# Kernel tuning notes

Measured on AMD Instinct MI355X. Metric: run time of the kernel, lower is better.

## Reference

```python
import jax, jax.numpy as jnp
import numpy as np

B, L, D, H, R = 2, 2048, 1024, 16, 32
DH = D // H
LORA_SCALE = 64.0 / 32.0  # alpha / rank


def _ln(x, w, b):
    mu = jnp.mean(x, axis=-1, keepdims=True)
    xc = x - mu
    var = jnp.mean(xc * xc, axis=-1, keepdims=True)
    y = xc * jax.lax.rsqrt(var + 1e-5) * w
    return y + b if b is not None else y


def _rotate_half(x):
    x1, x2 = jnp.split(x, 2, axis=-1)
    return jnp.concatenate([-x2, x1], axis=-1)


def _apply_rotary(q, k):
    # q, k: [B, L, H, DH]
    seqlen = q.shape[1]
    inv_freq = 1.0 / (10000.0 ** (jnp.arange(0, DH, 2, dtype=jnp.float32) / DH))
    t = jnp.arange(seqlen, dtype=jnp.float32)
    freqs = t[:, None] * inv_freq[None, :]           # [L, DH/2]
    emb = jnp.concatenate([freqs, freqs], axis=-1)   # [L, DH]
    cos = jnp.cos(emb)[None, :, None, :]
    sin = jnp.sin(emb)[None, :, None, :]
    q = q * cos + _rotate_half(q) * sin
    k = k * cos + _rotate_half(k) * sin
    return q, k


def setup_inputs() -> dict:
    key = jax.random.key(0)
    ks = jax.random.split(key, 10)
    s = 0.02
    return {
        "x": jax.random.normal(ks[0], (B, L, D), dtype=jnp.float32),
        "seq_id": jnp.sort(jax.random.randint(ks[1], (B, L), 0, 4), axis=-1),
        "ln_w": jnp.ones((D,), jnp.float32),
        "ln_b": jnp.zeros((D,), jnp.float32),
        "w_qkv": jax.random.normal(ks[2], (3 * D, D), jnp.float32) * s,
        "q_lora_a": jax.random.normal(ks[3], (R, D), jnp.float32) * s,
        "q_lora_b": jax.random.normal(ks[4], (D, R), jnp.float32) * s,
        "v_lora_a": jax.random.normal(ks[5], (R, D), jnp.float32) * s,
        "v_lora_b": jax.random.normal(ks[6], (D, R), jnp.float32) * s,
        "q_ln_w": jnp.ones((D,), jnp.float32),
        "k_ln_w": jnp.ones((D,), jnp.float32),
        "w_out": jax.random.normal(ks[7], (D, D), jnp.float32) * s,
    }


def reference(x, seq_id, ln_w, ln_b, w_qkv, q_lora_a, q_lora_b,
              v_lora_a, v_lora_b, q_ln_w, k_ln_w, w_out):
    h = _ln(x, ln_w, ln_b)                          # [B, L, D]
    qkv = jnp.einsum('bld,ed->ble', h, w_qkv)       # [B, L, 3D]
    q, k, v = jnp.split(qkv, 3, axis=-1)
    q = q + LORA_SCALE * jnp.einsum('blr,dr->bld', jnp.einsum('bld,rd->blr', h, q_lora_a), q_lora_b)
    v = v + LORA_SCALE * jnp.einsum('blr,dr->bld', jnp.einsum('bld,rd->blr', h, v_lora_a), v_lora_b)
    q = _ln(q, q_ln_w, None)
    k = _ln(k, k_ln_w, None)
    q = q.reshape(B, L, H, DH)
    k = k.reshape(B, L, H, DH)
    q, k = _apply_rotary(q, k)
    qh = q.transpose(0, 2, 1, 3)                    # [B, H, L, DH]
    kh = k.transpose(0, 2, 1, 3)
    vh = v.reshape(B, L, H, DH).transpose(0, 2, 1, 3)
    scale = 1.0 / np.sqrt(DH)
    scores = jnp.einsum('bhqd,bhkd->bhqk', qh, kh) * scale
    mask = (seq_id[:, None, :, None] == seq_id[:, None, None, :])  # [B,1,L,L]
    scores = jnp.where(mask, scores, jnp.finfo(scores.dtype).min)
    attn = jax.nn.softmax(scores, axis=-1)
    ctx = jnp.einsum('bhqk,bhkd->bhqd', attn, vh)   # [B, H, L, DH]
    ctx = ctx.transpose(0, 2, 1, 3).reshape(B, L, D)
    return jnp.einsum('bld,ed->ble', ctx, w_out)
```

## Files before the change

kernel.cpp:

```cpp
#include <hip/hip_runtime.h>
#include <hip/hip_bf16.h>
#include <cmath>

constexpr int Bb = 2;
constexpr int Ls = 2048;
constexpr int Dd = 1024;
constexpr int Hh = 16;
constexpr int DHh = 64;
constexpr int Rr = 32;
constexpr int BL = Bb * Ls;
constexpr float LORA_SCALE = 2.0f;
constexpr float LN_EPS = 1e-5f;
constexpr float ATTN_SCALE = 0.125f;
constexpr float LOG2E = 1.4426950408889634f;
constexpr float QSCL = ATTN_SCALE * LOG2E;

typedef __attribute__((ext_vector_type(8))) short bf16x8;
typedef __attribute__((ext_vector_type(4))) float f32x4;

__device__ __forceinline__ unsigned short f2bf(float f) {
    __hip_bfloat16 b = __float2bfloat16(f);
    return *reinterpret_cast<unsigned short*>(&b);
}
__device__ __forceinline__ float bf2f(unsigned short u) {
    unsigned int x = ((unsigned int)u) << 16;
    return __uint_as_float(x);
}
__device__ __forceinline__ void async_copy16(const void* g, void* l) {
    __builtin_amdgcn_global_load_lds(
        (__attribute__((address_space(1))) void*)(void*)(size_t)g,
        (__attribute__((address_space(3))) void*)l, 16, 0, 0);
}

__device__ __forceinline__ float block_sum_256(float v, float* red) {
#pragma unroll
    for (int o = 32; o > 0; o >>= 1) v += __shfl_down(v, o, 64);
    const int lane = threadIdx.x & 63;
    const int wid = threadIdx.x >> 6;
    if (lane == 0) red[wid] = v;
    __syncthreads();
    float s = red[0] + red[1] + red[2] + red[3];
    __syncthreads();
    return s;
}

__global__ __launch_bounds__(256) void prep_ln_kernel(const float* __restrict__ w,
                                                      const float* __restrict__ qa,
                                                      const float* __restrict__ qb,
                                                      const float* __restrict__ va,
                                                      const float* __restrict__ vb,
                                                      const float* __restrict__ wout,
                                                      const float* __restrict__ x,
                                                      const float* __restrict__ lnw,
                                                      const float* __restrict__ lnb,
                                                      unsigned short* __restrict__ wqkvb,
                                                      unsigned short* __restrict__ woutb,
                                                      float* __restrict__ ropec,
                                                      float* __restrict__ ropes,
                                                      unsigned short* __restrict__ hb) {
    const int blk = blockIdx.x;
    const int tid = threadIdx.x;
    if (blk < 3 * Dd) {
        const int e = blk;
        const int d0 = tid * 4;
        __shared__ float br[Rr];
        const bool isq = (e < Dd);
        const bool isv = (e >= 2 * Dd);
        const float* bsrc = isq ? (qb + (size_t)e * Rr)
                                : (isv ? (vb + (size_t)(e - 2 * Dd) * Rr) : nullptr);
        const float* asrc = isq ? qa : va;
        if (bsrc && tid < Rr) br[tid] = bsrc[tid];
        __syncthreads();
        float acc[4] = {0.f, 0.f, 0.f, 0.f};
        if (bsrc) {
#pragma unroll 8
            for (int r = 0; r < Rr; ++r) {
                float4 av = *(const float4*)(asrc + (size_t)r * Dd + d0);
                acc[0] += br[r] * av.x; acc[1] += br[r] * av.y;
                acc[2] += br[r] * av.z; acc[3] += br[r] * av.w;
            }
        }
        float4 wv = *(const float4*)(w + (size_t)e * Dd + d0);
        ushort4 o;
        o.x = f2bf(wv.x + LORA_SCALE * acc[0]);
        o.y = f2bf(wv.y + LORA_SCALE * acc[1]);
        o.z = f2bf(wv.z + LORA_SCALE * acc[2]);
        o.w = f2bf(wv.w + LORA_SCALE * acc[3]);
        *(ushort4*)(wqkvb + (size_t)e * Dd + d0) = o;
    } else if (blk < 4 * Dd) {
        int i = ((blk - 3 * Dd) * 256 + tid) * 4;
        float4 v = *(const float4*)(wout + i);
        ushort4 o;
        o.x = f2bf(v.x); o.y = f2bf(v.y); o.z = f2bf(v.z); o.w = f2bf(v.w);
        *(ushort4*)(woutb + i) = o;
    } else if (blk < 4 * Dd + 256) {
        int i = (blk - 4 * Dd) * 256 + tid;
        int l = i >> 5;
        int f = i & 31;
        float invf = powf(10000.0f, -(float)f * (1.0f / 32.0f));
        float ang = (float)l * invf;
        float s, c;
        sincosf(ang, &s, &c);
        ropec[i] = c;
        ropes[i] = s;
    } else {
        const int w64 = tid >> 6;
        const int L = tid & 63;
        const int row = (blk - (4 * Dd + 256)) * 4 + w64;
        const float* xr = x + (size_t)row * Dd;
        float4 v4[4];
        float v[16];
#pragma unroll
        for (int c = 0; c < 4; ++c) {
            v4[c] = *(const float4*)(xr + c * 256 + L * 4);
            v[c * 4 + 0] = v4[c].x; v[c * 4 + 1] = v4[c].y;
            v[c * 4 + 2] = v4[c].z; v[c * 4 + 3] = v4[c].w;
        }
        float s = 0.f;
#pragma unroll
        for (int j = 0; j < 16; ++j) s += v[j];
#pragma unroll
        for (int off = 1; off < 64; off <<= 1) s += __shfl_xor(s, off, 64);
        float mean = s * (1.0f / Dd);
        float sq = 0.f;
#pragma unroll
        for (int j = 0; j < 16; ++j) {
            v[j] -= mean;
            sq += v[j] * v[j];
        }
#pragma unroll
        for (int off = 1; off < 64; off <<= 1) sq += __shfl_xor(sq, off, 64);
        float rs = rsqrtf(sq * (1.0f / Dd) + LN_EPS);
        unsigned short* hr = hb + (size_t)row * Dd;
#pragma unroll
        for (int c = 0; c < 4; ++c) {
            int d = c * 256 + L * 4;
            float4 wv = *(const float4*)(lnw + d);
            float4 bv = *(const float4*)(lnb + d);
            ushort4 o;
            o.x = f2bf(v[c * 4 + 0] * rs * wv.x + bv.x);
            o.y = f2bf(v[c * 4 + 1] * rs * wv.y + bv.y);
            o.z = f2bf(v[c * 4 + 2] * rs * wv.z + bv.z);
            o.w = f2bf(v[c * 4 + 3] * rs * wv.w + bv.w);
            *(ushort4*)(hr + d) = o;
        }
    }
}

__global__ __launch_bounds__(256) void gemm_bt_mfma(const unsigned short* __restrict__ A,
                                                    const unsigned short* __restrict__ B,
                                                    unsigned short* __restrict__ C,
                                                    int M, int N, int K) {
    __shared__ short As[128 * 64];
    __shared__ short Bs[128 * 64];
    const int tid = threadIdx.x;
    const int w = tid >> 6, lane = tid & 63, quad = lane >> 4, l15 = lane & 15;
    const int m0 = blockIdx.y * 128, n0 = blockIdx.x * 128;
    const int wm = (w & 1) * 64, wn = (w >> 1) * 64;
    f32x4 acc[4][4];
#pragma unroll
    for (int i = 0; i < 4; ++i)
#pragma unroll
        for (int j = 0; j < 4; ++j) acc[i][j] = f32x4{0.f, 0.f, 0.f, 0.f};

    for (int k0 = 0; k0 < K; k0 += 64) {
#pragma unroll
        for (int j = 0; j < 4; ++j) {
            int c = tid + j * 256;
            int row = c >> 3;
            int jg = (c & 7) ^ (row & 7);
            async_copy16(A + (size_t)(m0 + row) * K + k0 + jg * 8, As + c * 8);
        }
#pragma unroll
        for (int j = 0; j < 4; ++j) {
            int c = tid + j * 256;
            int row = c >> 3;
            int jg = (c & 7) ^ (row & 7);
            async_copy16(B + (size_t)(n0 + row) * K + k0 + jg * 8, Bs + c * 8);
        }
        __syncthreads();
#pragma unroll
        for (int ks = 0; ks < 2; ++ks) {
            bf16x8 a[4], b[4];
#pragma unroll
            for (int mi = 0; mi < 4; ++mi) {
                int row = wm + mi * 16 + l15;
                int ch = (ks * 4 + quad) ^ (row & 7);
                a[mi] = *(const bf16x8*)&As[row * 64 + ch * 8];
            }
#pragma unroll
            for (int ni = 0; ni < 4; ++ni) {
                int row = wn + ni * 16 + l15;
                int ch = (ks * 4 + quad) ^ (row & 7);
                b[ni] = *(const bf16x8*)&Bs[row * 64 + ch * 8];
            }
#pragma unroll
            for (int mi = 0; mi < 4; ++mi)
#pragma unroll
                for (int ni = 0; ni < 4; ++ni)
                    acc[mi][ni] = __builtin_amdgcn_mfma_f32_16x16x32_bf16(a[mi], b[ni], acc[mi][ni], 0, 0, 0);
        }
        __syncthreads();
    }
#pragma unroll
    for (int mi = 0; mi < 4; ++mi)
#pragma unroll
        for (int ni = 0; ni < 4; ++ni)
#pragma unroll
            for (int r = 0; r < 4; ++r)
                C[(size_t)(m0 + wm + mi * 16 + quad * 4 + r) * N + n0 + wn + ni * 16 + l15] =
                    f2bf(acc[mi][ni][r]);
}

__global__ __launch_bounds__(256) void gemm_bt_mfma_n64(const unsigned short* __restrict__ A,
                                                        const unsigned short* __restrict__ B,
                                                        float* __restrict__ C,
                                                        int M, int N, int K) {
    __shared__ short As[128 * 64];
    __shared__ short Bs[64 * 64];
    const int tid = threadIdx.x;
    const int w = tid >> 6, lane = tid & 63, quad = lane >> 4, l15 = lane & 15;
    const int m0 = blockIdx.y * 128, n0 = blockIdx.x * 64;
    const int wm = (w & 1) * 64, wn = (w >> 1) * 32;
    f32x4 acc[4][2];
#pragma unroll
    for (int i = 0; i < 4; ++i)
#pragma unroll
        for (int j = 0; j < 2; ++j) acc[i][j] = f32x4{0.f, 0.f, 0.f, 0.f};

    for (int k0 = 0; k0 < K; k0 += 64) {
#pragma unroll
        for (int j = 0; j < 4; ++j) {
            int c = tid + j * 256;
            int row = c >> 3;
            int jg = (c & 7) ^ (row & 7);
            async_copy16(A + (size_t)(m0 + row) * K + k0 + jg * 8, As + c * 8);
        }
#pragma unroll
        for (int j = 0; j < 2; ++j) {
            int c = tid + j * 256;
            int row = c >> 3;
            int jg = (c & 7) ^ (row & 7);
            async_copy16(B + (size_t)(n0 + row) * K + k0 + jg * 8, Bs + c * 8);
        }
        __syncthreads();
#pragma unroll
        for (int ks = 0; ks < 2; ++ks) {
            bf16x8 a[4], b[2];
#pragma unroll
            for (int mi = 0; mi < 4; ++mi) {
                int row = wm + mi * 16 + l15;
                int ch = (ks * 4 + quad) ^ (row & 7);
                a[mi] = *(const bf16x8*)&As[row * 64 + ch * 8];
            }
#pragma unroll
            for (int ni = 0; ni < 2; ++ni) {
                int row = wn + ni * 16 + l15;
                int ch = (ks * 4 + quad) ^ (row & 7);
                b[ni] = *(const bf16x8*)&Bs[row * 64 + ch * 8];
            }
#pragma unroll
            for (int mi = 0; mi < 4; ++mi)
#pragma unroll
                for (int ni = 0; ni < 2; ++ni)
                    acc[mi][ni] = __builtin_amdgcn_mfma_f32_16x16x32_bf16(a[mi], b[ni], acc[mi][ni], 0, 0, 0);
        }
        __syncthreads();
    }
#pragma unroll
    for (int mi = 0; mi < 4; ++mi)
#pragma unroll
        for (int ni = 0; ni < 2; ++ni)
#pragma unroll
            for (int r = 0; r < 4; ++r)
                C[(size_t)(m0 + wm + mi * 16 + quad * 4 + r) * N + n0 + wn + ni * 16 + l15] =
                    acc[mi][ni][r];
}

__global__ __launch_bounds__(256) void qkv_final_kernel(const unsigned short* __restrict__ qkvb,
                                                        const float* __restrict__ qlnw,
                                                        const float* __restrict__ klnw,
                                                        const float* __restrict__ ropec,
                                                        const float* __restrict__ ropes,
                                                        unsigned short* __restrict__ qt,
                                                        unsigned short* __restrict__ kt,
                                                        unsigned short* __restrict__ vtt) {
    const int blk = blockIdx.x;
    const int tid = threadIdx.x;
    if (blk < BL / 4) {
        const int w64 = tid >> 6;
        const int L = tid & 63;
        const int row = blk * 4 + w64;
        const int b = row >> 11;
        const int l = row & (Ls - 1);
        const unsigned short* qp = qkvb + (size_t)row * (3 * Dd);
        const unsigned short* kp = qp + Dd;

        bf16x8 qA = *(const bf16x8*)(qp + L * 8);
        bf16x8 qB = *(const bf16x8*)(qp + 512 + L * 8);
        bf16x8 kA = *(const bf16x8*)(kp + L * 8);
        bf16x8 kB = *(const bf16x8*)(kp + 512 + L * 8);
        float vq[16], vk[16];
#pragma unroll
        for (int j = 0; j < 8; ++j) {
            vq[j] = bf2f((unsigned short)qA[j]);
            vq[8 + j] = bf2f((unsigned short)qB[j]);
            vk[j] = bf2f((unsigned short)kA[j]);
            vk[8 + j] = bf2f((unsigned short)kB[j]);
        }
        float sq = 0.f, sk = 0.f;
#pragma unroll
        for (int j = 0; j < 16; ++j) { sq += vq[j]; sk += vk[j]; }
#pragma unroll
        for (int off = 1; off < 64; off <<= 1) {
            sq += __shfl_xor(sq, off, 64);
            sk += __shfl_xor(sk, off, 64);
        }
        float mq = sq * (1.0f / Dd), mk = sk * (1.0f / Dd);
        float vvq = 0.f, vvk = 0.f;
#pragma unroll
        for (int j = 0; j < 16; ++j) {
            vq[j] -= mq; vvq += vq[j] * vq[j];
            vk[j] -= mk; vvk += vk[j] * vk[j];
        }
#pragma unroll
        for (int off = 1; off < 64; off <<= 1) {
            vvq += __shfl_xor(vvq, off, 64);
            vvk += __shfl_xor(vvk, off, 64);
        }
        float rsq = rsqrtf(vvq * (1.0f / Dd) + LN_EPS);
        float rsk = rsqrtf(vvk * (1.0f / Dd) + LN_EPS);

        float yq[16], yk[16];
        {
            float4 w0 = *(const float4*)(qlnw + L * 8);
            float4 w1 = *(const float4*)(qlnw + L * 8 + 4);
            float4 w2 = *(const float4*)(qlnw + 512 + L * 8);
            float4 w3 = *(const float4*)(qlnw + 512 + L * 8 + 4);
            yq[0] = vq[0] * rsq * w0.x; yq[1] = vq[1] * rsq * w0.y;
            yq[2] = vq[2] * rsq * w0.z; yq[3] = vq[3] * rsq * w0.w;
            yq[4] = vq[4] * rsq * w1.x; yq[5] = vq[5] * rsq * w1.y;
            yq[6] = vq[6] * rsq * w1.z; yq[7] = vq[7] * rsq * w1.w;
            yq[8] = vq[8] * rsq * w2.x; yq[9] = vq[9] * rsq * w2.y;
            yq[10] = vq[10] * rsq * w2.z; yq[11] = vq[11] * rsq * w2.w;
            yq[12] = vq[12] * rsq * w3.x; yq[13] = vq[13] * rsq * w3.y;
            yq[14] = vq[14] * rsq * w3.z; yq[15] = vq[15] * rsq * w3.w;
        }
        {
            float4 w0 = *(const float4*)(klnw + L * 8);
            float4 w1 = *(const float4*)(klnw + L * 8 + 4);
            float4 w2 = *(const float4*)(klnw + 512 + L * 8);
            float4 w3 = *(const float4*)(klnw + 512 + L * 8 + 4);
            yk[0] = vk[0] * rsk * w0.x; yk[1] = vk[1] * rsk * w0.y;
            yk[2] = vk[2] * rsk * w0.z; yk[3] = vk[3] * rsk * w0.w;
            yk[4] = vk[4] * rsk * w1.x; yk[5] = vk[5] * rsk * w1.y;
            yk[6] = vk[6] * rsk * w1.z; yk[7] = vk[7] * rsk * w1.w;
            yk[8] = vk[8] * rsk * w2.x; yk[9] = vk[9] * rsk * w2.y;
            yk[10] = vk[10] * rsk * w2.z; yk[11] = vk[11] * rsk * w2.w;
            yk[12] = vk[12] * rsk * w3.x; yk[13] = vk[13] * rsk * w3.y;
            yk[14] = vk[14] * rsk * w3.z; yk[15] = vk[15] * rsk * w3.w;
        }

        float cs[8], sn[8];
        {
            int fbase = l * 32 + (L & 3) * 8;
            float4 c0 = *(const float4*)(ropec + fbase);
            float4 c1 = *(const float4*)(ropec + fbase + 4);
            float4 s0 = *(const float4*)(ropes + fbase);
            float4 s1 = *(const float4*)(ropes + fbase + 4);
            cs[0] = c0.x; cs[1] = c0.y; cs[2] = c0.z; cs[3] = c0.w;
            cs[4] = c1.x; cs[5] = c1.y; cs[6] = c1.z; cs[7] = c1.w;
            sn[0] = s0.x; sn[1] = s0.y; sn[2] = s0.z; sn[3] = s0.w;
            sn[4] = s1.x; sn[5] = s1.y; sn[6] = s1.z; sn[7] = s1.w;
        }
        const float sgn = (L & 4) ? 1.0f : -1.0f;
        unsigned short outqA[8], outqB[8], outkA[8], outkB[8];
#pragma unroll
        for (int j = 0; j < 8; ++j) {
            float pA = __shfl_xor(yq[j], 4, 64);
            float pB = __shfl_xor(yq[8 + j], 4, 64);
            outqA[j] = f2bf((yq[j] * cs[j] + sgn * pA * sn[j]) * QSCL);
            outqB[j] = f2bf((yq[8 + j] * cs[j] + sgn * pB * sn[j]) * QSCL);
            float pkA = __shfl_xor(yk[j], 4, 64);
            float pkB = __shfl_xor(yk[8 + j], 4, 64);
            outkA[j] = f2bf(yk[j] * cs[j] + sgn * pkA * sn[j]);
            outkB[j] = f2bf(yk[8 + j] * cs[j] + sgn * pkB * sn[j]);
        }
        const int hA = L >> 3;
        const int dh0 = (L & 7) * 8;
        size_t offA = (((size_t)(b * Hh + hA)) * Ls + l) * DHh + dh0;
        size_t offB = (((size_t)(b * Hh + 8 + hA)) * Ls + l) * DHh + dh0;
        *(uint4*)(qt + offA) = *(uint4*)outqA;
        *(uint4*)(qt + offB) = *(uint4*)outqB;
        *(uint4*)(kt + offA) = *(uint4*)outkA;
        *(uint4*)(kt + offB) = *(uint4*)outkB;
    } else {
        const int t2 = blk - BL / 4;
        const int l0 = (t2 & 31) * 64;
        const int h = (t2 >> 5) & 15;
        const int b = t2 >> 9;
        __shared__ short t[64][72];
        const unsigned short* src = qkvb + (size_t)b * Ls * (3 * Dd) + 2 * Dd + h * 64;
#pragma unroll
        for (int j = 0; j < 2; ++j) {
            int g = tid + j * 256;
            int row = g >> 3;
            int c0 = (g & 7) * 8;
            uint4 vv = *(const uint4*)(src + (size_t)(l0 + row) * (3 * Dd) + c0);
            *(uint4*)&t[row][c0] = vv;
        }
        __syncthreads();
        unsigned short* dst = vtt + ((size_t)(b * Hh + h) * DHh) * Ls;
#pragma unroll
        for (int j = 0; j < 2; ++j) {
            int g = tid + j * 256;
            int dh = g >> 3;
            int lc = (g & 7) * 8;
            ushort4 o0, o1;
            unsigned short* p0 = (unsigned short*)&o0;
            unsigned short* p1 = (unsigned short*)&o1;
#pragma unroll
            for (int i = 0; i < 4; ++i) p0[i] = (unsigned short)t[lc + i][dh];
#pragma unroll
            for (int i = 0; i < 4; ++i) p1[i] = (unsigned short)t[lc + 4 + i][dh];
            *(ushort4*)(dst + (size_t)dh * Ls + l0 + lc) = o0;
            *(ushort4*)(dst + (size_t)dh * Ls + l0 + lc + 4) = o1;
        }
    }
}

constexpr int PSP = 76;

__global__ __launch_bounds__(256) void attn_kernel(const unsigned short* __restrict__ qt,
                                                   const unsigned short* __restrict__ kt,
                                                   const unsigned short* __restrict__ vtt,
                                                   const int* __restrict__ seq_id,
                                                   unsigned short* __restrict__ ctxb) {
    const int id = blockIdx.x;
    const int c8 = id & 7;
    const int x = (id >> 3) & 31;
    const int g4 = id >> 8;
    const int v = c8 + 8 * g4;
    const int b = v >> 4;
    const int h = v & 15;
    const int q0 = x * 64;

    const size_t base = ((size_t)(b * Hh + h)) * Ls * DHh;
    const size_t base_v = ((size_t)(b * Hh + h)) * DHh * Ls;
    const int* sid = seq_id + (size_t)b * Ls;

    __shared__ short Ks[2][64 * 64];
    __shared__ short Vs[2][64 * 64];
    __shared__ short Ps[4][16 * PSP];
    __shared__ int sq_s[64];

    const int tid = threadIdx.x;
    const int w = tid >> 6;
    const int lane = tid & 63;
    const int quad = lane >> 4;
    const int l15 = lane & 15;

    if (tid < 64) sq_s[tid] = sid[q0 + tid];
    const int qmin = sid[q0];
    const int qmax = sid[q0 + 63];

    bool need = false;
    if (lane < 32) {
        int kmn = sid[lane * 64];
        int kmx = sid[lane * 64 + 63];
        need = (kmn <= qmax) && (kmx >= qmin);
    }
    unsigned long long bmask = __ballot(need);
    const int t0 = __builtin_ctzll(bmask);
    const int t1 = 64 - __builtin_clzll(bmask);

    auto stage = [&](int buf, int t) {
#pragma unroll
        for (int j = 0; j < 2; ++j) {
            int cc = tid + j * 256;
            int row = cc >> 3;
            int jg = (cc & 7) ^ (row & 7);
            async_copy16(kt + base + (size_t)(t * 64 + row) * DHh + jg * 8,
                         &Ks[buf][cc * 8]);
            async_copy16(vtt + base_v + (size_t)row * Ls + t * 64 + jg * 8,
                         &Vs[buf][cc * 8]);
        }
    };

    stage(0, t0);
    const int qrow = q0 + w * 16 + l15;
    const bf16x8 a0 = *(const bf16x8*)(qt + base + (size_t)qrow * DHh + quad * 8);
    const bf16x8 a1 = *(const bf16x8*)(qt + base + (size_t)qrow * DHh + 32 + quad * 8);

    int sqv[4];
    float lsum[4] = {0.f, 0.f, 0.f, 0.f};
    f32x4 O[4];
#pragma unroll
    for (int r = 0; r < 4; ++r) O[r] = f32x4{0.f, 0.f, 0.f, 0.f};

    __syncthreads();
#pragma unroll
    for (int r = 0; r < 4; ++r) sqv[r] = sq_s[w * 16 + quad * 4 + r];

    for (int t = t0; t < t1; ++t) {
        const int cur = (t - t0) & 1;
        if (t + 1 < t1) stage(cur ^ 1, t + 1);
        const int k0 = t * 64;

        f32x4 s[4];
#pragma unroll
        for (int kg = 0; kg < 4; ++kg) {
            int krow = kg * 16 + l15;
            bf16x8 b0 = *(const bf16x8*)&Ks[cur][krow * 64 + ((0 + quad) ^ (krow & 7)) * 8];
            bf16x8 b1 = *(const bf16x8*)&Ks[cur][krow * 64 + ((4 + quad) ^ (krow & 7)) * 8];
            f32x4 acc = {0.f, 0.f, 0.f, 0.f};
            acc = __builtin_amdgcn_mfma_f32_16x16x32_bf16(a0, b0, acc, 0, 0, 0);
            acc = __builtin_amdgcn_mfma_f32_16x16x32_bf16(a1, b1, acc, 0, 0, 0);
            s[kg] = acc;
        }

        const int kmn = sid[k0];
        const int kmx = sid[k0 + 63];
        const bool nomask = (kmn == kmx) && (qmin == qmax) && (kmn == qmin);
        if (!nomask) {
#pragma unroll
            for (int kg = 0; kg < 4; ++kg) {
                int skv = sid[k0 + kg * 16 + l15];
#pragma unroll
                for (int r = 0; r < 4; ++r)
                    if (sqv[r] != skv) s[kg][r] = -3.0e38f;
            }
        }
#pragma unroll
        for (int kg = 0; kg < 4; ++kg)
#pragma unroll
            for (int r = 0; r < 4; ++r)
                s[kg][r] = __builtin_amdgcn_exp2f(s[kg][r]);
#pragma unroll
        for (int r = 0; r < 4; ++r)
            lsum[r] += s[0][r] + s[1][r] + s[2][r] + s[3][r];

#pragma unroll
        for (int kg = 0; kg < 4; ++kg)
#pragma unroll
            for (int r = 0; r < 4; ++r)
                Ps[w][(quad * 4 + r) * PSP + kg * 16 + l15] = (short)f2bf(s[kg][r]);

        bf16x8 pa0 = *(const bf16x8*)&Ps[w][l15 * PSP + quad * 8];
        bf16x8 pa1 = *(const bf16x8*)&Ps[w][l15 * PSP + 32 + quad * 8];
#pragma unroll
        for (int ng = 0; ng < 4; ++ng) {
            int vrow = ng * 16 + l15;
            bf16x8 vb0 = *(const bf16x8*)&Vs[cur][vrow * 64 + ((0 + quad) ^ (vrow & 7)) * 8];
            bf16x8 vb1 = *(const bf16x8*)&Vs[cur][vrow * 64 + ((4 + quad) ^ (vrow & 7)) * 8];
            O[ng] = __builtin_amdgcn_mfma_f32_16x16x32_bf16(pa0, vb0, O[ng], 0, 0, 0);
            O[ng] = __builtin_amdgcn_mfma_f32_16x16x32_bf16(pa1, vb1, O[ng], 0, 0, 0);
        }

        __syncthreads();
    }

#pragma unroll
    for (int off = 1; off < 16; off <<= 1)
#pragma unroll
        for (int r = 0; r < 4; ++r)
            lsum[r] += __shfl_xor(lsum[r], off, 64);
    float inv_l[4];
#pragma unroll
    for (int r = 0; r < 4; ++r) inv_l[r] = 1.0f / lsum[r];
#pragma unroll
    for (int ng = 0; ng < 4; ++ng)
#pragma unroll
        for (int r = 0; r < 4; ++r) {
            int q = q0 + w * 16 + quad * 4 + r;
            ctxb[((size_t)b * Ls + q) * Dd + h * DHh + ng * 16 + l15] =
                f2bf(O[ng][r] * inv_l[r]);
        }
}

extern "C" void kernel_launch(void* const* d_in, const int* in_sizes, int n_in,
                              void* d_out, int out_size, void* d_ws, size_t ws_size,
                              hipStream_t stream) {
    const float* x = (const float*)d_in[0];
    const int* seq_id = (const int*)d_in[1];
    const float* ln_w = (const float*)d_in[2];
    const float* ln_b = (const float*)d_in[3];
    const float* w_qkv = (const float*)d_in[4];
    const float* q_lora_a = (const float*)d_in[5];
    const float* q_lora_b = (const float*)d_in[6];
    const float* v_lora_a = (const float*)d_in[7];
    const float* v_lora_b = (const float*)d_in[8];
    const float* q_ln_w = (const float*)d_in[9];
    const float* k_ln_w = (const float*)d_in[10];
    const float* w_out = (const float*)d_in[11];
    float* out = (float*)d_out;

    const size_t SZ = (size_t)BL * Dd;
    float* p = (float*)d_ws;
    float* ropec = p;          p += (size_t)Ls * 32;
    float* ropes = p;          p += (size_t)Ls * 32;
    unsigned short* ub = (unsigned short*)p;
    unsigned short* qkvb = ub; ub += 3 * SZ;
    unsigned short* hb = ub;   ub += SZ;
    unsigned short* qt = ub;   ub += SZ;
    unsigned short* kt = ub;   ub += SZ;
    unsigned short* vtt = ub;  ub += SZ;
    unsigned short* ctxb = ub; ub += SZ;
    unsigned short* wqkvb = ub; ub += (size_t)3 * Dd * Dd;
    unsigned short* woutb = ub; ub += (size_t)Dd * Dd;

    prep_ln_kernel<<<4 * Dd + 256 + BL / 4, 256, 0, stream>>>(
        w_qkv, q_lora_a, q_lora_b, v_lora_a, v_lora_b, w_out,
        x, ln_w, ln_b, wqkvb, woutb, ropec, ropes, hb);
    {
        dim3 g(3 * Dd / 128, BL / 128);
        gemm_bt_mfma<<<g, 256, 0, stream>>>(hb, wqkvb, qkvb, BL, 3 * Dd, Dd);
    }
    qkv_final_kernel<<<BL / 4 + 1024, 256, 0, stream>>>(qkvb, q_ln_w, k_ln_w,
                                                        ropec, ropes, qt, kt, vtt);
    attn_kernel<<<1024, 256, 0, stream>>>(qt, kt, vtt, seq_id, ctxb);
    {
        dim3 g(Dd / 64, BL / 128);
        gemm_bt_mfma_n64<<<g, 256, 0, stream>>>(ctxb, woutb, out, BL, Dd, Dd);
    }
}
```

Baseline: 204.2 us.

## Schedule attention tiles dynamically with an atomic work queue; widen out-proj tile

```diff
diff --git a/kernel.cpp b/kernel.cpp
--- a/kernel.cpp
+++ b/kernel.cpp
@@ -30,18 +30,6 @@
     __builtin_amdgcn_global_load_lds(
         (__attribute__((address_space(1))) void*)(void*)(size_t)g,
         (__attribute__((address_space(3))) void*)l, 16, 0, 0);
-}
-
-__device__ __forceinline__ float block_sum_256(float v, float* red) {
-#pragma unroll
-    for (int o = 32; o > 0; o >>= 1) v += __shfl_down(v, o, 64);
-    const int lane = threadIdx.x & 63;
-    const int wid = threadIdx.x >> 6;
-    if (lane == 0) red[wid] = v;
-    __syncthreads();
-    float s = red[0] + red[1] + red[2] + red[3];
-    __syncthreads();
-    return s;
 }
 
 __global__ __launch_bounds__(256) void prep_ln_kernel(const float* __restrict__ w,
@@ -212,21 +200,21 @@
                     f2bf(acc[mi][ni][r]);
 }
 
-__global__ __launch_bounds__(256) void gemm_bt_mfma_n64(const unsigned short* __restrict__ A,
+__global__ __launch_bounds__(256) void gemm_bt_mfma_f32(const unsigned short* __restrict__ A,
                                                         const unsigned short* __restrict__ B,
                                                         float* __restrict__ C,
                                                         int M, int N, int K) {
     __shared__ short As[128 * 64];
-    __shared__ short Bs[64 * 64];
+    __shared__ short Bs[128 * 64];
     const int tid = threadIdx.x;
     const int w = tid >> 6, lane = tid & 63, quad = lane >> 4, l15 = lane & 15;
-    const int m0 = blockIdx.y * 128, n0 = blockIdx.x * 64;
-    const int wm = (w & 1) * 64, wn = (w >> 1) * 32;
-    f32x4 acc[4][2];
+    const int m0 = blockIdx.y * 128, n0 = blockIdx.x * 128;
+    const int wm = (w & 1) * 64, wn = (w >> 1) * 64;
+    f32x4 acc[4][4];
 #pragma unroll
     for (int i = 0; i < 4; ++i)
 #pragma unroll
-        for (int j = 0; j < 2; ++j) acc[i][j] = f32x4{0.f, 0.f, 0.f, 0.f};
+        for (int j = 0; j < 4; ++j) acc[i][j] = f32x4{0.f, 0.f, 0.f, 0.f};
 
     for (int k0 = 0; k0 < K; k0 += 64) {
 #pragma unroll
@@ -237,7 +225,7 @@
             async_copy16(A + (size_t)(m0 + row) * K + k0 + jg * 8, As + c * 8);
         }
 #pragma unroll
-        for (int j = 0; j < 2; ++j) {
+        for (int j = 0; j < 4; ++j) {
             int c = tid + j * 256;
             int row = c >> 3;
             int jg = (c & 7) ^ (row & 7);
@@ -246,7 +234,7 @@
         __syncthreads();
 #pragma unroll
         for (int ks = 0; ks < 2; ++ks) {
-            bf16x8 a[4], b[2];
+            bf16x8 a[4], b[4];
 #pragma unroll
             for (int mi = 0; mi < 4; ++mi) {
                 int row = wm + mi * 16 + l15;
@@ -254,7 +242,7 @@
                 a[mi] = *(const bf16x8*)&As[row * 64 + ch * 8];
             }
 #pragma unroll
-            for (int ni = 0; ni < 2; ++ni) {
+            for (int ni = 0; ni < 4; ++ni) {
                 int row = wn + ni * 16 + l15;
                 int ch = (ks * 4 + quad) ^ (row & 7);
                 b[ni] = *(const bf16x8*)&Bs[row * 64 + ch * 8];
@@ -262,7 +250,7 @@
 #pragma unroll
             for (int mi = 0; mi < 4; ++mi)
 #pragma unroll
-                for (int ni = 0; ni < 2; ++ni)
+                for (int ni = 0; ni < 4; ++ni)
                     acc[mi][ni] = __builtin_amdgcn_mfma_f32_16x16x32_bf16(a[mi], b[ni], acc[mi][ni], 0, 0, 0);
         }
         __syncthreads();
@@ -270,7 +258,7 @@
 #pragma unroll
     for (int mi = 0; mi < 4; ++mi)
 #pragma unroll
-        for (int ni = 0; ni < 2; ++ni)
+        for (int ni = 0; ni < 4; ++ni)
 #pragma unroll
             for (int r = 0; r < 4; ++r)
                 C[(size_t)(m0 + wm + mi * 16 + quad * 4 + r) * N + n0 + wn + ni * 16 + l15] =
@@ -284,9 +272,11 @@
                                                         const float* __restrict__ ropes,
                                                         unsigned short* __restrict__ qt,
                                                         unsigned short* __restrict__ kt,
-                                                        unsigned short* __restrict__ vtt) {
+                                                        unsigned short* __restrict__ vtt,
+                                                        int* __restrict__ wq) {
     const int blk = blockIdx.x;
     const int tid = threadIdx.x;
+    if (blk == 0 && tid == 0) *wq = 512;
     if (blk < BL / 4) {
         const int w64 = tid >> 6;
         const int L = tid & 63;
@@ -435,24 +425,13 @@
                                                    const unsigned short* __restrict__ kt,
                                                    const unsigned short* __restrict__ vtt,
                                                    const int* __restrict__ seq_id,
-                                                   unsigned short* __restrict__ ctxb) {
-    const int id = blockIdx.x;
-    const int c8 = id & 7;
-    const int x = (id >> 3) & 31;
-    const int g4 = id >> 8;
-    const int v = c8 + 8 * g4;
-    const int b = v >> 4;
-    const int h = v & 15;
-    const int q0 = x * 64;
-
-    const size_t base = ((size_t)(b * Hh + h)) * Ls * DHh;
-    const size_t base_v = ((size_t)(b * Hh + h)) * DHh * Ls;
-    const int* sid = seq_id + (size_t)b * Ls;
-
+                                                   unsigned short* __restrict__ ctxb,
+                                                   int* __restrict__ wq) {
     __shared__ short Ks[2][64 * 64];
     __shared__ short Vs[2][64 * 64];
     __shared__ short Ps[4][16 * PSP];
     __shared__ int sq_s[64];
+    __shared__ int item_s;
 
     const int tid = threadIdx.x;
     const int w = tid >> 6;
@@ -460,122 +439,139 @@
     const int quad = lane >> 4;
     const int l15 = lane & 15;
 
-    if (tid < 64) sq_s[tid] = sid[q0 + tid];
-    const int qmin = sid[q0];
-    const int qmax = sid[q0 + 63];
-
-    bool need = false;
-    if (lane < 32) {
-        int kmn = sid[lane * 64];
-        int kmx = sid[lane * 64 + 63];
-        need = (kmn <= qmax) && (kmx >= qmin);
+    int it = blockIdx.x;
+    while (it < 1024) {
+        const int v = it >> 5;
+        const int x = it & 31;
+        const int b = v >> 4;
+        const int h = v & 15;
+        const int q0 = x * 64;
+
+        const size_t base = ((size_t)(b * Hh + h)) * Ls * DHh;
+        const size_t base_v = ((size_t)(b * Hh + h)) * DHh * Ls;
+        const int* sid = seq_id + (size_t)b * Ls;
+
+        if (tid < 64) sq_s[tid] = sid[q0 + tid];
+        const int qmin = sid[q0];
+        const int qmax = sid[q0 + 63];
+
+        bool need = false;
+        if (lane < 32) {
+            int kmn = sid[lane * 64];
+            int kmx = sid[lane * 64 + 63];
+            need = (kmn <= qmax) && (kmx >= qmin);
+        }
+        unsigned long long bmask = __ballot(need);
+        const int t0 = __builtin_ctzll(bmask);
+        const int t1 = 64 - __builtin_clzll(bmask);
+
+        auto stage = [&](int buf, int t) {
+#pragma unroll
+            for (int j = 0; j < 2; ++j) {
+                int cc = tid + j * 256;
+                int row = cc >> 3;
+                int jg = (cc & 7) ^ (row & 7);
+                async_copy16(kt + base + (size_t)(t * 64 + row) * DHh + jg * 8,
+                             &Ks[buf][cc * 8]);
+                async_copy16(vtt + base_v + (size_t)row * Ls + t * 64 + jg * 8,
+                             &Vs[buf][cc * 8]);
+            }
+        };
+
+        stage(0, t0);
+        const int qrow = q0 + w * 16 + l15;
+        const bf16x8 a0 = *(const bf16x8*)(qt + base + (size_t)qrow * DHh + quad * 8);
+        const bf16x8 a1 = *(const bf16x8*)(qt + base + (size_t)qrow * DHh + 32 + quad * 8);
+
+        int sqv[4];
+        float lsum[4] = {0.f, 0.f, 0.f, 0.f};
+        f32x4 O[4];
+#pragma unroll
+        for (int r = 0; r < 4; ++r) O[r] = f32x4{0.f, 0.f, 0.f, 0.f};
+
+        __syncthreads();
+#pragma unroll
+        for (int r = 0; r < 4; ++r) sqv[r] = sq_s[w * 16 + quad * 4 + r];
+
+        for (int t = t0; t < t1; ++t) {
+            const int cur = (t - t0) & 1;
+            if (t + 1 < t1) stage(cur ^ 1, t + 1);
+            const int k0 = t * 64;
+
+            f32x4 s[4];
+#pragma unroll
+            for (int kg = 0; kg < 4; ++kg) {
+                int krow = kg * 16 + l15;
+                bf16x8 b0 = *(const bf16x8*)&Ks[cur][krow * 64 + ((0 + quad) ^ (krow & 7)) * 8];
+                bf16x8 b1 = *(const bf16x8*)&Ks[cur][krow * 64 + ((4 + quad) ^ (krow & 7)) * 8];
+                f32x4 acc = {0.f, 0.f, 0.f, 0.f};
+                acc = __builtin_amdgcn_mfma_f32_16x16x32_bf16(a0, b0, acc, 0, 0, 0);
+                acc = __builtin_amdgcn_mfma_f32_16x16x32_bf16(a1, b1, acc, 0, 0, 0);
+                s[kg] = acc;
+            }
+
+            const int kmn = sid[k0];
+            const int kmx = sid[k0 + 63];
+            const bool nomask = (kmn == kmx) && (qmin == qmax) && (kmn == qmin);
+            if (!nomask) {
+#pragma unroll
+                for (int kg = 0; kg < 4; ++kg) {
+                    int skv = sid[k0 + kg * 16 + l15];
+#pragma unroll
+                    for (int r = 0; r < 4; ++r)
+                        if (sqv[r] != skv) s[kg][r] = -3.0e38f;
+                }
+            }
+#pragma unroll
+            for (int kg = 0; kg < 4; ++kg)
+#pragma unroll
+                for (int r = 0; r < 4; ++r)
+                    s[kg][r] = __builtin_amdgcn_exp2f(s[kg][r]);
+#pragma unroll
+            for (int r = 0; r < 4; ++r)
+                lsum[r] += s[0][r] + s[1][r] + s[2][r] + s[3][r];
+
+#pragma unroll
+            for (int kg = 0; kg < 4; ++kg)
+#pragma unroll
+                for (int r = 0; r < 4; ++r)
+                    Ps[w][(quad * 4 + r) * PSP + kg * 16 + l15] = (short)f2bf(s[kg][r]);
+
+            bf16x8 pa0 = *(const bf16x8*)&Ps[w][l15 * PSP + quad * 8];
+            bf16x8 pa1 = *(const bf16x8*)&Ps[w][l15 * PSP + 32 + quad * 8];
+#pragma unroll
+            for (int ng = 0; ng < 4; ++ng) {
+                int vrow = ng * 16 + l15;
+                bf16x8 vb0 = *(const bf16x8*)&Vs[cur][vrow * 64 + ((0 + quad) ^ (vrow & 7)) * 8];
+                bf16x8 vb1 = *(const bf16x8*)&Vs[cur][vrow * 64 + ((4 + quad) ^ (vrow & 7)) * 8];
+                O[ng] = __builtin_amdgcn_mfma_f32_16x16x32_bf16(pa0, vb0, O[ng], 0, 0, 0);
+                O[ng] = __builtin_amdgcn_mfma_f32_16x16x32_bf16(pa1, vb1, O[ng], 0, 0, 0);
+            }
+
+            __syncthreads();
+        }
+
+#pragma unroll
+        for (int off = 1; off < 16; off <<= 1)
+#pragma unroll
+            for (int r = 0; r < 4; ++r)
+                lsum[r] += __shfl_xor(lsum[r], off, 64);
+        float inv_l[4];
+#pragma unroll
+        for (int r = 0; r < 4; ++r) inv_l[r] = 1.0f / lsum[r];
+#pragma unroll
+        for (int ng = 0; ng < 4; ++ng)
+#pragma unroll
+            for (int r = 0; r < 4; ++r) {
+                int q = q0 + w * 16 + quad * 4 + r;
+                ctxb[((size_t)b * Ls + q) * Dd + h * DHh + ng * 16 + l15] =
+                    f2bf(O[ng][r] * inv_l[r]);
+            }
+
+        if (tid == 0) item_s = atomicAdd(wq, 1);
+        __syncthreads();
+        it = item_s;
     }
-    unsigned long long bmask = __ballot(need);
-    const int t0 = __builtin_ctzll(bmask);
-    const int t1 = 64 - __builtin_clzll(bmask);
-
-    auto stage = [&](int buf, int t) {
-#pragma unroll
-        for (int j = 0; j < 2; ++j) {
-            int cc = tid + j * 256;
-            int row = cc >> 3;
-            int jg = (cc & 7) ^ (row & 7);
-            async_copy16(kt + base + (size_t)(t * 64 + row) * DHh + jg * 8,
-                         &Ks[buf][cc * 8]);
-            async_copy16(vtt + base_v + (size_t)row * Ls + t * 64 + jg * 8,
-                         &Vs[buf][cc * 8]);
-        }
-    };
-
-    stage(0, t0);
-    const int qrow = q0 + w * 16 + l15;
-    const bf16x8 a0 = *(const bf16x8*)(qt + base + (size_t)qrow * DHh + quad * 8);
-    const bf16x8 a1 = *(const bf16x8*)(qt + base + (size_t)qrow * DHh + 32 + quad * 8);
-
-    int sqv[4];
-    float lsum[4] = {0.f, 0.f, 0.f, 0.f};
-    f32x4 O[4];
-#pragma unroll
-    for (int r = 0; r < 4; ++r) O[r] = f32x4{0.f, 0.f, 0.f, 0.f};
-
-    __syncthreads();
-#pragma unroll
-    for (int r = 0; r < 4; ++r) sqv[r] = sq_s[w * 16 + quad * 4 + r];
-
-    for (int t = t0; t < t1; ++t) {
-        const int cur = (t - t0) & 1;
-        if (t + 1 < t1) stage(cur ^ 1, t + 1);
-        const int k0 = t * 64;
-
-        f32x4 s[4];
-#pragma unroll
-        for (int kg = 0; kg < 4; ++kg) {
-            int krow = kg * 16 + l15;
-            bf16x8 b0 = *(const bf16x8*)&Ks[cur][krow * 64 + ((0 + quad) ^ (krow & 7)) * 8];
-            bf16x8 b1 = *(const bf16x8*)&Ks[cur][krow * 64 + ((4 + quad) ^ (krow & 7)) * 8];
-            f32x4 acc = {0.f, 0.f, 0.f, 0.f};
-            acc = __builtin_amdgcn_mfma_f32_16x16x32_bf16(a0, b0, acc, 0, 0, 0);
-            acc = __builtin_amdgcn_mfma_f32_16x16x32_bf16(a1, b1, acc, 0, 0, 0);
-            s[kg] = acc;
-        }
-
-        const int kmn = sid[k0];
-        const int kmx = sid[k0 + 63];
-        const bool nomask = (kmn == kmx) && (qmin == qmax) && (kmn == qmin);
-        if (!nomask) {
-#pragma unroll
-            for (int kg = 0; kg < 4; ++kg) {
-                int skv = sid[k0 + kg * 16 + l15];
-#pragma unroll
-                for (int r = 0; r < 4; ++r)
-                    if (sqv[r] != skv) s[kg][r] = -3.0e38f;
-            }
-        }
-#pragma unroll
-        for (int kg = 0; kg < 4; ++kg)
-#pragma unroll
-            for (int r = 0; r < 4; ++r)
-                s[kg][r] = __builtin_amdgcn_exp2f(s[kg][r]);
-#pragma unroll
-        for (int r = 0; r < 4; ++r)
-            lsum[r] += s[0][r] + s[1][r] + s[2][r] + s[3][r];
-
-#pragma unroll
-        for (int kg = 0; kg < 4; ++kg)
-#pragma unroll
-            for (int r = 0; r < 4; ++r)
-                Ps[w][(quad * 4 + r) * PSP + kg * 16 + l15] = (short)f2bf(s[kg][r]);
-
-        bf16x8 pa0 = *(const bf16x8*)&Ps[w][l15 * PSP + quad * 8];
-        bf16x8 pa1 = *(const bf16x8*)&Ps[w][l15 * PSP + 32 + quad * 8];
-#pragma unroll
-        for (int ng = 0; ng < 4; ++ng) {
-            int vrow = ng * 16 + l15;
-            bf16x8 vb0 = *(const bf16x8*)&Vs[cur][vrow * 64 + ((0 + quad) ^ (vrow & 7)) * 8];
-            bf16x8 vb1 = *(const bf16x8*)&Vs[cur][vrow * 64 + ((4 + quad) ^ (vrow & 7)) * 8];
-            O[ng] = __builtin_amdgcn_mfma_f32_16x16x32_bf16(pa0, vb0, O[ng], 0, 0, 0);
-            O[ng] = __builtin_amdgcn_mfma_f32_16x16x32_bf16(pa1, vb1, O[ng], 0, 0, 0);
-        }
-
-        __syncthreads();
-    }
-
-#pragma unroll
-    for (int off = 1; off < 16; off <<= 1)
-#pragma unroll
-        for (int r = 0; r < 4; ++r)
-            lsum[r] += __shfl_xor(lsum[r], off, 64);
-    float inv_l[4];
-#pragma unroll
-    for (int r = 0; r < 4; ++r) inv_l[r] = 1.0f / lsum[r];
-#pragma unroll
-    for (int ng = 0; ng < 4; ++ng)
-#pragma unroll
-        for (int r = 0; r < 4; ++r) {
-            int q = q0 + w * 16 + quad * 4 + r;
-            ctxb[((size_t)b * Ls + q) * Dd + h * DHh + ng * 16 + l15] =
-                f2bf(O[ng][r] * inv_l[r]);
-        }
 }
 
 extern "C" void kernel_launch(void* const* d_in, const int* in_sizes, int n_in,
@@ -608,6 +604,7 @@
     unsigned short* ctxb = ub; ub += SZ;
     unsigned short* wqkvb = ub; ub += (size_t)3 * Dd * Dd;
     unsigned short* woutb = ub; ub += (size_t)Dd * Dd;
+    int* wq = (int*)ub;        ub += 64;
 
     prep_ln_kernel<<<4 * Dd + 256 + BL / 4, 256, 0, stream>>>(
         w_qkv, q_lora_a, q_lora_b, v_lora_a, v_lora_b, w_out,
@@ -617,10 +614,10 @@
         gemm_bt_mfma<<<g, 256, 0, stream>>>(hb, wqkvb, qkvb, BL, 3 * Dd, Dd);
     }
     qkv_final_kernel<<<BL / 4 + 1024, 256, 0, stream>>>(qkvb, q_ln_w, k_ln_w,
-                                                        ropec, ropes, qt, kt, vtt);
-    attn_kernel<<<1024, 256, 0, stream>>>(qt, kt, vtt, seq_id, ctxb);
+                                                        ropec, ropes, qt, kt, vtt, wq);
+    attn_kernel<<<512, 256, 0, stream>>>(qt, kt, vtt, seq_id, ctxb, wq);
     {
-        dim3 g(Dd / 64, BL / 128);
-        gemm_bt_mfma_n64<<<g, 256, 0, stream>>>(ctxb, woutb, out, BL, Dd, Dd);
+        dim3 g(Dd / 128, BL / 128);
+        gemm_bt_mfma_f32<<<g, 256, 0, stream>>>(ctxb, woutb, out, BL, Dd, Dd);
     }
 }
```

Result: slower. 222.5 us (+9.0%).
